# Optimization experiments

Measured on AMD Instinct MI355X. Metric: run time of the kernel, lower is better.

## Reference

```python
import jax, jax.numpy as jnp
import numpy as np

# Config (matches init_kwargs): range [-32,32]^3, voxel 0.5 -> 128^3 grid; BEV 200x200
PC_LOW = np.array([-32.0, -32.0, -32.0], dtype=np.float32)
PC_HIGH = np.array([32.0, 32.0, 32.0], dtype=np.float32)
VOX = 0.5
G = 128
BEV_H, BEV_W = 200, 200
BN_EPS = 1e-5
STRIDES = [1, 2, 1, 2, 1, 1]


def setup_inputs() -> dict:
    key = jax.random.key(0)
    ks = jax.random.split(key, 10)
    N = 2_000_000
    xyz = jax.random.uniform(ks[0], (N, 3), jnp.float32, minval=-32.0, maxval=32.0)
    inten = jax.random.uniform(ks[1], (N, 1), jnp.float32)
    points = jnp.concatenate([xyz, inten], axis=1)  # (N,4)
    chans = [(32, 4), (64, 32), (64, 64), (128, 64), (128, 128), (256, 128)]
    inp = {"points": points}
    for i, (co, ci) in enumerate(chans):
        fan_in = ci * 27
        inp[f"w{i+1}"] = jax.random.normal(ks[2 + i], (co, ci, 3, 3, 3), jnp.float32) / np.sqrt(fan_in)
        inp[f"g{i+1}"] = jnp.ones((co,), jnp.float32)
        inp[f"b{i+1}"] = jnp.zeros((co,), jnp.float32)
    return inp


def _voxelize(points):
    # range filtering + floor-binning + clamp, faithful to voxelize_points (dense path: scatter-ADD)
    low = jnp.asarray(PC_LOW)
    high = jnp.asarray(PC_HIGH)
    mask = jnp.all((points[:, :3] >= low) & (points[:, :3] <= high), axis=1)
    coords = jnp.floor((points[:, :3] - low) / VOX).astype(jnp.int32)
    coords = jnp.clip(coords, 0, G - 1)
    vals = points * mask[:, None].astype(points.dtype)  # invalid points contribute 0
    # original indexes voxel_grid[:, z, y, x]
    grid = jnp.zeros((G, G, G, 4), points.dtype)
    grid = grid.at[coords[:, 2], coords[:, 1], coords[:, 0]].add(vals)
    return jnp.transpose(grid, (3, 0, 1, 2))  # (4, G, G, G)


def _conv3d(x, w, s):
    # PyTorch Conv3d(k=3, padding=1, stride=s), NCDHW
    return jax.lax.conv_general_dilated(
        x, w, window_strides=(s, s, s), padding=[(1, 1), (1, 1), (1, 1)],
        dimension_numbers=("NCDHW", "OIDHW", "NCDHW"))


def _bn_relu(x, g, b):
    # eval-mode BN: running_mean=0, running_var=1
    scale = (g / jnp.sqrt(1.0 + BN_EPS))[None, :, None, None, None]
    return jax.nn.relu(x * scale + b[None, :, None, None, None])


def reference(points, w1, w2, w3, w4, w5, w6,
              g1, g2, g3, g4, g5, g6,
              b1, b2, b3, b4, b5, b6):
    ws = [w1, w2, w3, w4, w5, w6]
    gs = [g1, g2, g3, g4, g5, g6]
    bs = [b1, b2, b3, b4, b5, b6]
    x = _voxelize(points)[None]  # (1,4,G,G,G)
    for w, g, b, s in zip(ws, gs, bs, STRIDES):
        x = _bn_relu(_conv3d(x, w, s), g, b)
    feat = x[0]  # (256, G/4, G/4, G/4)
    bev = jnp.max(feat, axis=2)  # torch.max(..., dim=2) on (C,D1,D2,D3) -> (C,D1,D3)
    # F.interpolate bilinear align_corners=False == jax.image.resize half-pixel bilinear
    bev = jax.image.resize(bev, (bev.shape[0], BEV_H, BEV_W), method="bilinear")
    return bev
```

## Files before the change

### kernel.cpp

```cpp
#include <hip/hip_runtime.h>
#include <hip/hip_fp16.h>
#include <cstdint>
#include <cstddef>

typedef __attribute__((ext_vector_type(8))) short short8;
typedef __attribute__((ext_vector_type(8))) _Float16 half8;
typedef __attribute__((ext_vector_type(16))) float f32x16;

__device__ __forceinline__ float bf2f(unsigned short u) { return __uint_as_float(((unsigned)u) << 16); }
__device__ __forceinline__ unsigned short f2bf(float f) {
    unsigned u = __float_as_uint(f);
    return (unsigned short)((u + 0x7fffu + ((u >> 16) & 1u)) >> 16);
}
__device__ __forceinline__ void sync_lds() {
    asm volatile("s_waitcnt lgkmcnt(0)\n\ts_barrier" ::: "memory");
}

static constexpr float BN_INV = 0.9999950000374997f;


__device__ __forceinline__ int vox_bucket(float4 p, bool& ok) {
    ok = !(p.x < -32.f || p.x > 32.f || p.y < -32.f || p.y > 32.f || p.z < -32.f || p.z > 32.f);
    int cy = min(max((int)floorf((p.y + 32.f) * 2.f), 0), 127);
    int cz = min(max((int)floorf((p.z + 32.f) * 2.f), 0), 127);
    return cz * 4 + (cy >> 5);
}

__global__ __launch_bounds__(256) void vox_count(const float4* __restrict__ pts,
                                                 int* __restrict__ cnt, int N) {
    __shared__ int h[512];
    for (int t = threadIdx.x; t < 512; t += 256) h[t] = 0;
    __syncthreads();
    int stride = gridDim.x * 256;
    for (int i = blockIdx.x * 256 + threadIdx.x; i < N; i += stride) {
        float4 p = pts[i];
        bool ok;
        int bk = vox_bucket(p, ok);
        if (ok) atomicAdd(&h[bk], 1);
    }
    __syncthreads();
    for (int t = threadIdx.x; t < 512; t += 256)
        if (h[t]) atomicAdd(&cnt[t], h[t]);
}

__global__ void vox_scan(const int* __restrict__ cnt, int* __restrict__ off,
                         int* __restrict__ cur) {
    __shared__ int c[512];
    int t = threadIdx.x;
    c[t] = cnt[t];
    __syncthreads();
    int s = 0;
    for (int i = 0; i < t; ++i) s += c[i];
    off[t] = s;
    cur[t] = s;
}

__global__ __launch_bounds__(256) void vox_scatter(const float4* __restrict__ pts,
                                                   int* __restrict__ cur,
                                                   float4* __restrict__ sorted, int N) {
    __shared__ int h[512];
    __shared__ int base[512];
    int b0 = blockIdx.x * 4096;
    for (int t = threadIdx.x; t < 512; t += 256) h[t] = 0;
    __syncthreads();
    float4 p[16];
    int bk[16];
#pragma unroll
    for (int j = 0; j < 16; ++j) {
        int i = b0 + j * 256 + threadIdx.x;
        bk[j] = -1;
        if (i < N) {
            p[j] = pts[i];
            bool ok;
            int b = vox_bucket(p[j], ok);
            if (ok) {
                bk[j] = b;
                atomicAdd(&h[b], 1);
            }
        }
    }
    __syncthreads();
    for (int t = threadIdx.x; t < 512; t += 256) {
        int n = h[t];
        base[t] = n ? atomicAdd(&cur[t], n) : 0;
        h[t] = 0;
    }
    __syncthreads();
#pragma unroll
    for (int j = 0; j < 16; ++j) {
        if (bk[j] >= 0) {
            int r = atomicAdd(&h[bk[j]], 1);
            sorted[base[bk[j]] + r] = p[j];
        }
    }
}

__global__ __launch_bounds__(256) void vox_accum(const float4* __restrict__ sorted,
                                                 const int* __restrict__ off,
                                                 const int* __restrict__ cnt,
                                                 __half2* __restrict__ grid) {
    __shared__ float s[32 * 128 * 4];
    for (int t = threadIdx.x; t < 16384; t += 256) s[t] = 0.f;
    __syncthreads();
    int bid = blockIdx.x;
    int bz = bid >> 2;
    int ylo = (bid & 3) << 5;
    int b = off[bid], n = cnt[bid];
    for (int i = threadIdx.x; i < n; i += 256) {
        float4 p = sorted[b + i];
        int cx = min(max((int)floorf((p.x + 32.f) * 2.f), 0), 127);
        int cy = min(max((int)floorf((p.y + 32.f) * 2.f), 0), 127);
        float* v = s + ((cy - ylo) * 128 + cx) * 4;
        unsafeAtomicAdd(v + 0, p.x);
        unsafeAtomicAdd(v + 1, p.y);
        unsafeAtomicAdd(v + 2, p.z);
        unsafeAtomicAdd(v + 3, p.w);
    }
    __syncthreads();
    for (int t = threadIdx.x; t < 4096; t += 256) {
        int ry = t >> 7, cx = t & 127;
        const float* v = s + t * 4;
        union { __half2 h[2]; float2 f; } u;
        u.h[0] = __floats2half2_rn(v[0], v[1]);
        u.h[1] = __floats2half2_rn(v[2], v[3]);
        int gi = (((bz + 1) * 130 + (ylo + ry + 1)) * 130 + (cx + 1)) * 2;
        *(float2*)(grid + gi) = u.f;
    }
}

__global__ __launch_bounds__(256) void repack_w(const float* __restrict__ w, const float* __restrict__ g,
                                                unsigned short* __restrict__ o, int Co, int CI) {
    int i = blockIdx.x * 256 + threadIdx.x;
    int total = 27 * Co * CI;
    if (i >= total) return;
    int ci = i % CI;
    int t = i / CI;
    int co = t % Co;
    int k = t / Co;
    float v = w[((size_t)(co * CI + ci)) * 27 + k] * g[co] * BN_INV;
    o[i] = f2bf(v);
}
__global__ __launch_bounds__(256) void repack_w1m(const float* __restrict__ w, const float* __restrict__ g,
                                                  unsigned short* __restrict__ o) {
    int i = blockIdx.x * 256 + threadIdx.x;
    if (i >= 9 * 32 * 16) return;
    int k16 = i & 15;
    int co = (i >> 4) & 31;
    int p = i >> 9;
    float v = 0.f;
    if (k16 < 12) {
        int dx = k16 >> 2, ci = k16 & 3;
        int dz = p / 3, dy = p % 3;
        v = w[(co * 4 + ci) * 27 + dz * 9 + dy * 3 + dx] * g[co] * BN_INV;
    }
    o[i] = __half_as_ushort(__float2half(v));
}

__global__ __launch_bounds__(256) void conv1_mfma(
    const unsigned short* __restrict__ in, const unsigned short* __restrict__ wa,
    const float* __restrict__ beta, unsigned short* __restrict__ out,
    int zstart, int r0) {
    const int tid = threadIdx.x;
    const int l31 = tid & 31;
    const int lh = (tid >> 5) & 1;
    const int wv = tid >> 6;
    int v = blockIdx.x * 128 + wv * 32 + l31;
    int x = v & 127;
    int y = (v >> 7) & 127;
    int z = zstart + (v >> 14);

    const unsigned short* base = in + ((z * 130 + y) * 130 + x) * 4 + lh * 8;
    uint2 d0[9], d1[9];
    half8 a[9];
#pragma unroll
    for (int p = 0; p < 9; ++p) {
        int dz = p / 3, dy = p % 3;
        const unsigned short* rp = base + (dz * 130 + dy) * 520;
        d0[p] = *(const uint2*)(rp);
        d1[p] = *(const uint2*)(rp + 4);
        a[p] = *(const half8*)(wa + (p * 32 + l31) * 16 + lh * 8);
    }
    f32x16 acc = {0.f};
#pragma unroll
    for (int p = 0; p < 9; ++p) {
        uint4 braw = {d0[p].x, d0[p].y, d1[p].x, d1[p].y};
        half8 b = *(half8*)&braw;
        acc = __builtin_amdgcn_mfma_f32_32x32x16_f16(a[p], b, acc, 0, 0, 0);
    }
    int r = z - zstart + r0;
    int ob = ((r * 130 + (y + 1)) * 130 + (x + 1)) * 32;
#pragma unroll
    for (int g = 0; g < 4; ++g) {
        int cb = 4 * lh + 8 * g;
        float4 bt = *(const float4*)(beta + cb);
        ushort4 u;
        u.x = f2bf(fmaxf(acc[g * 4 + 0] + bt.x, 0.f));
        u.y = f2bf(fmaxf(acc[g * 4 + 1] + bt.y, 0.f));
        u.z = f2bf(fmaxf(acc[g * 4 + 2] + bt.z, 0.f));
        u.w = f2bf(fmaxf(acc[g * 4 + 3] + bt.w, 0.f));
        *(ushort4*)(out + ob + cb) = u;
    }
}

template <int CI, int KC, int S>
__global__ __launch_bounds__(256) void conv_mfma(
    const unsigned short* __restrict__ in, const unsigned short* __restrict__ wb,
    const float* __restrict__ beta, unsigned short* __restrict__ out,
    int D, int lgD, int Xp, int Xpo, int Co, int zin_base, int v_off) {

    constexpr int KCp = KC + 8;
    constexpr int OPB = KC / 8;
    constexpr int NB = KC / 16;
    constexpr int NA = KC / 32;
    constexpr int NCH = KC / 16;
    constexpr int NCC = CI / KC;
    constexpr int STOT = 27 * NCC;

    __shared__ __align__(16) short sA[2 * 64 * KCp];
    __shared__ __align__(16) short sB[2 * 128 * KCp];

    const int tid = threadIdx.x;
    const int l31 = tid & 31;
    const int lh = (tid >> 5) & 1;
    const int wv = tid >> 6;

    const unsigned gx = gridDim.x;
    const unsigned lin = blockIdx.y * gx + blockIdx.x;
    const unsigned q = (gx * gridDim.y) >> 3;
    const unsigned lin2 = (lin & 7) * q + (lin >> 3);
    const unsigned bxs = lin2 % gx;
    const unsigned bys = lin2 / gx;
    const int co0 = bxs * 64;

    int bgIdx[NB], blB[NB];
#pragma unroll
    for (int j = 0; j < NB; ++j) {
        int idx = tid + j * 256;
        int vL = idx / OPB;
        int oct = idx - vL * OPB;
        int vg = v_off + bys * 128 + vL;
        int x = vg & (D - 1);
        int ry = vg >> lgD;
        int y = ry & (D - 1);
        int z = ry >> lgD;
        bgIdx[j] = ((z * S * Xp + y * S) * Xp + x * S) * CI + oct * 8;
        blB[j] = vL * KCp + oct * 8;
    }
    int agIdx[NA], alA[NA];
#pragma unroll
    for (int j = 0; j < NA; ++j) {
        int idx = tid + j * 256;
        int cA = idx / OPB;
        int oct = idx - cA * OPB;
        agIdx[j] = (co0 + cA) * CI + oct * 8;
        alA[j] = cA * KCp + oct * 8;
    }
    const int bfr = (wv * 32 + l31) * KCp + lh * 8;
    const int afr = l31 * KCp + lh * 8;

    short8 rB[2][NB], rA[2][NA];

    auto loadStage = [&](int s, int r) {
        int k = s / NCC;
        int c0 = (s - k * NCC) * KC;
        int dz = k / 9;
        int rr = k - dz * 9;
        int dy = rr / 3;
        int dx = rr - dy * 3;
        int kb = (((dz - zin_base) * Xp + dy) * Xp + dx) * CI + c0;
        int ka = k * Co * CI + c0;
#pragma unroll
        for (int j = 0; j < NB; ++j) rB[r][j] = *(const short8*)(in + bgIdx[j] + kb);
#pragma unroll
        for (int j = 0; j < NA; ++j) rA[r][j] = *(const short8*)(wb + agIdx[j] + ka);
    };
    auto storeLDS = [&](int r, int buf) {
#pragma unroll
        for (int j = 0; j < NB; ++j) *(short8*)(sB + buf * 128 * KCp + blB[j]) = rB[r][j];
#pragma unroll
        for (int j = 0; j < NA; ++j) *(short8*)(sA + buf * 64 * KCp + alA[j]) = rA[r][j];
    };

    f32x16 acc0 = {0.f}, acc1 = {0.f};

    loadStage(0, 0);
    loadStage(1, 1);
    storeLDS(0, 0);
    sync_lds();

#pragma unroll
    for (int s = 0; s < STOT; ++s) {
        if (s + 2 < STOT) loadStage(s + 2, s & 1);
        const short* pB = sB + (s & 1) * 128 * KCp + bfr;
        const short* pA = sA + (s & 1) * 64 * KCp + afr;
#pragma unroll
        for (int c = 0; c < NCH; ++c) {
            short8 bv = *(const short8*)(pB + c * 16);
            short8 a0 = *(const short8*)(pA + c * 16);
            short8 a1 = *(const short8*)(pA + 32 * KCp + c * 16);
            acc0 = __builtin_amdgcn_mfma_f32_32x32x16_bf16(a0, bv, acc0, 0, 0, 0);
            acc1 = __builtin_amdgcn_mfma_f32_32x32x16_bf16(a1, bv, acc1, 0, 0, 0);
        }
        if (s + 1 < STOT) {
            storeLDS((s + 1) & 1, (s + 1) & 1);
            sync_lds();
        }
    }

    int vg = v_off + bys * 128 + wv * 32 + l31;
    int x = vg & (D - 1);
    int ry = vg >> lgD;
    int y = ry & (D - 1);
    int z = ry >> lgD;
    size_t ob = (((size_t)(z + 1) * Xpo + (y + 1)) * Xpo + (x + 1)) * Co + co0;
#pragma unroll
    for (int cot = 0; cot < 2; ++cot) {
        const f32x16& a = cot ? acc1 : acc0;
#pragma unroll
        for (int g = 0; g < 4; ++g) {
            int cb = cot * 32 + 4 * lh + 8 * g;
            float4 bt = *(const float4*)(beta + co0 + cb);
            ushort4 u;
            u.x = f2bf(fmaxf(a[g * 4 + 0] + bt.x, 0.f));
            u.y = f2bf(fmaxf(a[g * 4 + 1] + bt.y, 0.f));
            u.z = f2bf(fmaxf(a[g * 4 + 2] + bt.z, 0.f));
            u.w = f2bf(fmaxf(a[g * 4 + 3] + bt.w, 0.f));
            *(ushort4*)(out + ob + cb) = u;
        }
    }
}

__global__ __launch_bounds__(256) void bev_max_kernel(const unsigned short* __restrict__ feat,
                                                      float* __restrict__ bev) {
    int z = blockIdx.x >> 5;
    int x = blockIdx.x & 31;
    int c = threadIdx.x;
    const unsigned short* p = feat + ((((z + 1) * 34) + 1) * 34 + (x + 1)) * 256 + c;
    float mx = 0.f;
#pragma unroll
    for (int y = 0; y < 32; ++y) mx = fmaxf(mx, bf2f(p[y * 34 * 256]));
    bev[(z * 32 + x) * 256 + c] = mx;
}

__global__ __launch_bounds__(256) void resize_kernel(const float* __restrict__ bev,
                                                     float* __restrict__ out) {
    int i = blockIdx.x * 256 + threadIdx.x;
    if (i >= 256 * 200 * 200) return;
    int ox = i % 200;
    int t = i / 200;
    int oy = t % 200;
    int c = t / 200;
    const float sc = 32.0f / 200.0f;
    float fy = (oy + 0.5f) * sc - 0.5f;
    float fx = (ox + 0.5f) * sc - 0.5f;
    float fy0 = floorf(fy), fx0 = floorf(fx);
    float ty = fy - fy0, tx = fx - fx0;
    int y0 = min(max((int)fy0, 0), 31), y1 = min(max((int)fy0 + 1, 0), 31);
    int x0 = min(max((int)fx0, 0), 31), x1 = min(max((int)fx0 + 1, 0), 31);
    float v00 = bev[(y0 * 32 + x0) * 256 + c], v01 = bev[(y0 * 32 + x1) * 256 + c];
    float v10 = bev[(y1 * 32 + x0) * 256 + c], v11 = bev[(y1 * 32 + x1) * 256 + c];
    float top = v00 + tx * (v01 - v00);
    float bot = v10 + tx * (v11 - v10);
    out[i] = top + ty * (bot - top);
}

extern "C" void kernel_launch(void* const* d_in, const int* in_sizes, int n_in,
                              void* d_out, int out_size, void* d_ws, size_t ws_size,
                              hipStream_t stream) {
    const float* points = (const float*)d_in[0];
    int N = in_sizes[0] / 4;
    const float *W[6], *G[6], *B[6];
    for (int i = 0; i < 6; ++i) {
        W[i] = (const float*)d_in[1 + 3 * i];
        G[i] = (const float*)d_in[2 + 3 * i];
        B[i] = (const float*)d_in[3 + 3 * i];
    }

    char* ws = (char*)d_ws;
    const size_t MiB = 1ull << 20;
    unsigned short* gridH = (unsigned short*)(ws);
    int* cnt = (int*)(ws + 17580032);
    int* off = cnt + 512;
    int* cur = off + 512;
    float4* sorted = (float4*)(ws + 18 * MiB);
    unsigned short* O1s = (unsigned short*)(ws + 18 * MiB);
    unsigned short* O2p = (unsigned short*)(ws + 104 * MiB);
    unsigned short* O3p = (unsigned short*)(ws);
    unsigned short* O4p = (unsigned short*)(ws + 37 * MiB);
    unsigned short* O5p = (unsigned short*)(ws + 48 * MiB);
    unsigned short* O6p = (unsigned short*)(ws + 59 * MiB);
    float* bev = (float*)(ws + 80 * MiB);
    unsigned short* wc1 = (unsigned short*)(ws + 140 * MiB);
    unsigned short* wb2 = (unsigned short*)(ws + 140 * MiB + 16384);
    unsigned short* wb3 = wb2 + 27 * 64 * 32;
    unsigned short* wb4 = wb3 + 27 * 64 * 64;
    unsigned short* wb5 = wb4 + 27 * 128 * 64;
    unsigned short* wb6 = wb5 + 27 * 128 * 128;

    repack_w1m<<<18, 256, 0, stream>>>(W[0], G[0], wc1);
    repack_w<<<216, 256, 0, stream>>>(W[1], G[1], wb2, 64, 32);
    repack_w<<<432, 256, 0, stream>>>(W[2], G[2], wb3, 64, 64);
    repack_w<<<864, 256, 0, stream>>>(W[3], G[3], wb4, 128, 64);
    repack_w<<<1728, 256, 0, stream>>>(W[4], G[4], wb5, 128, 128);
    repack_w<<<3456, 256, 0, stream>>>(W[5], G[5], wb6, 256, 128);

    hipMemsetAsync(gridH, 0, 17576000, stream);
    hipMemsetAsync(cnt, 0, 2048, stream);
    hipMemsetAsync(O2p, 0, 36799488, stream);
    vox_count<<<1024, 256, 0, stream>>>((const float4*)points, cnt, N);
    vox_scan<<<1, 512, 0, stream>>>(cnt, off, cur);
    vox_scatter<<<(N + 4095) / 4096, 256, 0, stream>>>((const float4*)points, cur, sorted, N);
    vox_accum<<<512, 256, 0, stream>>>(sorted, off, cnt, (__half2*)gridH);

    hipMemsetAsync(O1s, 0, 70304000, stream);
    conv1_mfma<<<8192, 256, 0, stream>>>(gridH, wc1, B[0], O1s, 0, 1);
    conv_mfma<32, 32, 2><<<dim3(1, 1024), 256, 0, stream>>>(O1s, wb2, B[1], O2p, 64, 6, 130, 66, 64, 0, 0);
    conv1_mfma<<<8320, 256, 0, stream>>>(gridH, wc1, B[0], O1s, 63, 0);
    conv_mfma<32, 32, 2><<<dim3(1, 1024), 256, 0, stream>>>(O1s, wb2, B[1], O2p, 64, 6, 130, 66, 64, 64, 131072);

    hipMemsetAsync(O3p, 0, 36799488, stream);
    hipMemsetAsync(O4p, 0, 10061824, stream);
    hipMemsetAsync(O5p, 0, 10061824, stream);
    hipMemsetAsync(O6p, 0, 20123648, stream);

    conv_mfma<64, 64, 1><<<dim3(1, 2048), 256, 0, stream>>>(O2p, wb3, B[2], O3p, 64, 6, 66, 66, 64, 0, 0);
    conv_mfma<64, 64, 2><<<dim3(2, 256), 256, 0, stream>>>(O3p, wb4, B[3], O4p, 32, 5, 66, 34, 128, 0, 0);
    conv_mfma<128, 64, 1><<<dim3(2, 256), 256, 0, stream>>>(O4p, wb5, B[4], O5p, 32, 5, 34, 34, 128, 0, 0);
    conv_mfma<128, 64, 1><<<dim3(4, 256), 256, 0, stream>>>(O5p, wb6, B[5], O6p, 32, 5, 34, 34, 256, 0, 0);

    bev_max_kernel<<<1024, 256, 0, stream>>>(O6p, bev);
    resize_kernel<<<40000, 256, 0, stream>>>(bev, (float*)d_out);
}
```

Before: 686.7 us.

## Enlarge conv tiles to 64x64 per wave with 2x2 MFMA register blocking

Generalizes the implicit-GEMM conv kernel to template block sizes over output channels and voxels. Each wave now computes a 64x64 tile with four accumulators, reusing each A and B fragment twice, and the K chunk is fixed at 32. Layers get larger blocks (e.g. 64x256 or 128x128), halving grid sizes, plus launch-bounds occupancy hints and partial unrolling for long stage loops. The aim is fewer LDS reads and global loads per MFMA; the cost is more registers, less occupancy and fewer blocks, which may hurt small layers.

```diff
diff --git a/kernel.cpp b/kernel.cpp
--- a/kernel.cpp
+++ b/kernel.cpp
@@ -202,27 +202,30 @@
     }
 }
 
-template <int CI, int KC, int S>
-__global__ __launch_bounds__(256) void conv_mfma(
+template <int CI, int BCO, int BVX, int S, int MINW>
+__global__ __launch_bounds__(256, MINW) void conv_mfma(
     const unsigned short* __restrict__ in, const unsigned short* __restrict__ wb,
     const float* __restrict__ beta, unsigned short* __restrict__ out,
     int D, int lgD, int Xp, int Xpo, int Co, int zin_base, int v_off) {
 
+    constexpr int KC = 32;
     constexpr int KCp = KC + 8;
     constexpr int OPB = KC / 8;
-    constexpr int NB = KC / 16;
-    constexpr int NA = KC / 32;
-    constexpr int NCH = KC / 16;
+    constexpr int NB = BVX * KC / (256 * 8);
+    constexpr int NA = BCO * KC / (256 * 8);
     constexpr int NCC = CI / KC;
     constexpr int STOT = 27 * NCC;
-
-    __shared__ __align__(16) short sA[2 * 64 * KCp];
-    __shared__ __align__(16) short sB[2 * 128 * KCp];
+    constexpr int WVX = BVX / 64;
+
+    __shared__ __align__(16) short sA[2 * BCO * KCp];
+    __shared__ __align__(16) short sB[2 * BVX * KCp];
 
     const int tid = threadIdx.x;
     const int l31 = tid & 31;
     const int lh = (tid >> 5) & 1;
     const int wv = tid >> 6;
+    const int voxW = (wv & (WVX - 1)) * 64;
+    const int coW = (wv / WVX) * 64;
 
     const unsigned gx = gridDim.x;
     const unsigned lin = blockIdx.y * gx + blockIdx.x;
@@ -230,7 +233,7 @@
     const unsigned lin2 = (lin & 7) * q + (lin >> 3);
     const unsigned bxs = lin2 % gx;
     const unsigned bys = lin2 / gx;
-    const int co0 = bxs * 64;
+    const int co0 = bxs * BCO;
 
     int bgIdx[NB], blB[NB];
 #pragma unroll
@@ -238,7 +241,7 @@
         int idx = tid + j * 256;
         int vL = idx / OPB;
         int oct = idx - vL * OPB;
-        int vg = v_off + bys * 128 + vL;
+        int vg = v_off + bys * BVX + vL;
         int x = vg & (D - 1);
         int ry = vg >> lgD;
         int y = ry & (D - 1);
@@ -255,8 +258,8 @@
         agIdx[j] = (co0 + cA) * CI + oct * 8;
         alA[j] = cA * KCp + oct * 8;
     }
-    const int bfr = (wv * 32 + l31) * KCp + lh * 8;
-    const int afr = l31 * KCp + lh * 8;
+    const int aoff = (coW + l31) * KCp + lh * 8;
+    const int boff = (voxW + l31) * KCp + lh * 8;
 
     short8 rB[2][NB], rA[2][NA];
 
@@ -276,56 +279,69 @@
     };
     auto storeLDS = [&](int r, int buf) {
 #pragma unroll
-        for (int j = 0; j < NB; ++j) *(short8*)(sB + buf * 128 * KCp + blB[j]) = rB[r][j];
-#pragma unroll
-        for (int j = 0; j < NA; ++j) *(short8*)(sA + buf * 64 * KCp + alA[j]) = rA[r][j];
+        for (int j = 0; j < NB; ++j) *(short8*)(sB + buf * BVX * KCp + blB[j]) = rB[r][j];
+#pragma unroll
+        for (int j = 0; j < NA; ++j) *(short8*)(sA + buf * BCO * KCp + alA[j]) = rA[r][j];
     };
 
-    f32x16 acc0 = {0.f}, acc1 = {0.f};
+    f32x16 acc00 = {0.f}, acc01 = {0.f}, acc10 = {0.f}, acc11 = {0.f};
 
     loadStage(0, 0);
     loadStage(1, 1);
     storeLDS(0, 0);
     sync_lds();
 
-#pragma unroll
-    for (int s = 0; s < STOT; ++s) {
+    auto stage = [&](int s) {
         if (s + 2 < STOT) loadStage(s + 2, s & 1);
-        const short* pB = sB + (s & 1) * 128 * KCp + bfr;
-        const short* pA = sA + (s & 1) * 64 * KCp + afr;
-#pragma unroll
-        for (int c = 0; c < NCH; ++c) {
-            short8 bv = *(const short8*)(pB + c * 16);
-            short8 a0 = *(const short8*)(pA + c * 16);
-            short8 a1 = *(const short8*)(pA + 32 * KCp + c * 16);
-            acc0 = __builtin_amdgcn_mfma_f32_32x32x16_bf16(a0, bv, acc0, 0, 0, 0);
-            acc1 = __builtin_amdgcn_mfma_f32_32x32x16_bf16(a1, bv, acc1, 0, 0, 0);
+        const short* pB = sB + (s & 1) * BVX * KCp;
+        const short* pA = sA + (s & 1) * BCO * KCp;
+#pragma unroll
+        for (int c = 0; c < 2; ++c) {
+            short8 a0 = *(const short8*)(pA + aoff + c * 16);
+            short8 a1 = *(const short8*)(pA + aoff + 32 * KCp + c * 16);
+            short8 b0 = *(const short8*)(pB + boff + c * 16);
+            short8 b1 = *(const short8*)(pB + boff + 32 * KCp + c * 16);
+            acc00 = __builtin_amdgcn_mfma_f32_32x32x16_bf16(a0, b0, acc00, 0, 0, 0);
+            acc01 = __builtin_amdgcn_mfma_f32_32x32x16_bf16(a0, b1, acc01, 0, 0, 0);
+            acc10 = __builtin_amdgcn_mfma_f32_32x32x16_bf16(a1, b0, acc10, 0, 0, 0);
+            acc11 = __builtin_amdgcn_mfma_f32_32x32x16_bf16(a1, b1, acc11, 0, 0, 0);
         }
         if (s + 1 < STOT) {
             storeLDS((s + 1) & 1, (s + 1) & 1);
             sync_lds();
         }
-    }
-
-    int vg = v_off + bys * 128 + wv * 32 + l31;
-    int x = vg & (D - 1);
-    int ry = vg >> lgD;
-    int y = ry & (D - 1);
-    int z = ry >> lgD;
-    size_t ob = (((size_t)(z + 1) * Xpo + (y + 1)) * Xpo + (x + 1)) * Co + co0;
-#pragma unroll
-    for (int cot = 0; cot < 2; ++cot) {
-        const f32x16& a = cot ? acc1 : acc0;
-#pragma unroll
-        for (int g = 0; g < 4; ++g) {
-            int cb = cot * 32 + 4 * lh + 8 * g;
-            float4 bt = *(const float4*)(beta + co0 + cb);
-            ushort4 u;
-            u.x = f2bf(fmaxf(a[g * 4 + 0] + bt.x, 0.f));
-            u.y = f2bf(fmaxf(a[g * 4 + 1] + bt.y, 0.f));
-            u.z = f2bf(fmaxf(a[g * 4 + 2] + bt.z, 0.f));
-            u.w = f2bf(fmaxf(a[g * 4 + 3] + bt.w, 0.f));
-            *(ushort4*)(out + ob + cb) = u;
+    };
+    if constexpr (STOT <= 54) {
+#pragma unroll
+        for (int s = 0; s < STOT; ++s) stage(s);
+    } else {
+#pragma unroll 2
+        for (int s = 0; s < STOT; ++s) stage(s);
+    }
+
+#pragma unroll
+    for (int i = 0; i < 2; ++i) {
+#pragma unroll
+        for (int j = 0; j < 2; ++j) {
+            const f32x16& a = (i == 0) ? (j == 0 ? acc00 : acc01) : (j == 0 ? acc10 : acc11);
+            int vg2 = v_off + bys * BVX + voxW + j * 32 + l31;
+            int x = vg2 & (D - 1);
+            int ry = vg2 >> lgD;
+            int y = ry & (D - 1);
+            int z = ry >> lgD;
+            int cbase = co0 + coW + i * 32;
+            size_t ob = (((size_t)(z + 1) * Xpo + (y + 1)) * Xpo + (x + 1)) * Co + cbase;
+#pragma unroll
+            for (int g = 0; g < 4; ++g) {
+                int cb = 4 * lh + 8 * g;
+                float4 bt = *(const float4*)(beta + cbase + cb);
+                ushort4 u;
+                u.x = f2bf(fmaxf(a[g * 4 + 0] + bt.x, 0.f));
+                u.y = f2bf(fmaxf(a[g * 4 + 1] + bt.y, 0.f));
+                u.z = f2bf(fmaxf(a[g * 4 + 2] + bt.z, 0.f));
+                u.w = f2bf(fmaxf(a[g * 4 + 3] + bt.w, 0.f));
+                *(ushort4*)(out + ob + cb) = u;
+            }
         }
     }
 }
@@ -414,19 +430,19 @@
 
     hipMemsetAsync(O1s, 0, 70304000, stream);
     conv1_mfma<<<8192, 256, 0, stream>>>(gridH, wc1, B[0], O1s, 0, 1);
-    conv_mfma<32, 32, 2><<<dim3(1, 1024), 256, 0, stream>>>(O1s, wb2, B[1], O2p, 64, 6, 130, 66, 64, 0, 0);
+    conv_mfma<32, 64, 256, 2, 3><<<dim3(1, 512), 256, 0, stream>>>(O1s, wb2, B[1], O2p, 64, 6, 130, 66, 64, 0, 0);
     conv1_mfma<<<8320, 256, 0, stream>>>(gridH, wc1, B[0], O1s, 63, 0);
-    conv_mfma<32, 32, 2><<<dim3(1, 1024), 256, 0, stream>>>(O1s, wb2, B[1], O2p, 64, 6, 130, 66, 64, 64, 131072);
+    conv_mfma<32, 64, 256, 2, 3><<<dim3(1, 512), 256, 0, stream>>>(O1s, wb2, B[1], O2p, 64, 6, 130, 66, 64, 64, 131072);
 
     hipMemsetAsync(O3p, 0, 36799488, stream);
     hipMemsetAsync(O4p, 0, 10061824, stream);
     hipMemsetAsync(O5p, 0, 10061824, stream);
     hipMemsetAsync(O6p, 0, 20123648, stream);
 
-    conv_mfma<64, 64, 1><<<dim3(1, 2048), 256, 0, stream>>>(O2p, wb3, B[2], O3p, 64, 6, 66, 66, 64, 0, 0);
-    conv_mfma<64, 64, 2><<<dim3(2, 256), 256, 0, stream>>>(O3p, wb4, B[3], O4p, 32, 5, 66, 34, 128, 0, 0);
-    conv_mfma<128, 64, 1><<<dim3(2, 256), 256, 0, stream>>>(O4p, wb5, B[4], O5p, 32, 5, 34, 34, 128, 0, 0);
-    conv_mfma<128, 64, 1><<<dim3(4, 256), 256, 0, stream>>>(O5p, wb6, B[5], O6p, 32, 5, 34, 34, 256, 0, 0);
+    conv_mfma<64, 64, 256, 1, 3><<<dim3(1, 1024), 256, 0, stream>>>(O2p, wb3, B[2], O3p, 64, 6, 66, 66, 64, 0, 0);
+    conv_mfma<64, 128, 128, 2, 4><<<dim3(1, 256), 256, 0, stream>>>(O3p, wb4, B[3], O4p, 32, 5, 66, 34, 128, 0, 0);
+    conv_mfma<128, 128, 128, 1, 4><<<dim3(1, 256), 256, 0, stream>>>(O4p, wb5, B[4], O5p, 32, 5, 34, 34, 128, 0, 0);
+    conv_mfma<128, 128, 128, 1, 4><<<dim3(2, 256), 256, 0, stream>>>(O5p, wb6, B[5], O6p, 32, 5, 34, 34, 256, 0, 0);
 
     bev_max_kernel<<<1024, 256, 0, stream>>>(O6p, bev);
     resize_kernel<<<40000, 256, 0, stream>>>(bev, (float*)d_out);
```

Result: slower. 746.6 us (+8.7%).

## Load activation B-fragments directly from global into registers, bypassing LDS

Applied to the files above, without the earlier changes.

The conv_mfma kernel no longer stages input activations through shared memory. Each lane now reads its own voxel's channel fragments straight from global memory into registers and feeds them to MFMA, which removes the sB buffer and its LDS stores and reads. Only weights still go through LDS. A launch-bounds occupancy hint of 4 blocks is also added. In exchange, global reads are per-lane strided, 16-byte accesses with no cooperative coalescing, and B prefetch depth drops to one stage.

```diff
diff --git a/kernel.cpp b/kernel.cpp
--- a/kernel.cpp
+++ b/kernel.cpp
@@ -203,21 +203,19 @@
 }
 
 template <int CI, int KC, int S>
-__global__ __launch_bounds__(256) void conv_mfma(
+__global__ __launch_bounds__(256, 4) void conv_mfma(
     const unsigned short* __restrict__ in, const unsigned short* __restrict__ wb,
     const float* __restrict__ beta, unsigned short* __restrict__ out,
     int D, int lgD, int Xp, int Xpo, int Co, int zin_base, int v_off) {
 
     constexpr int KCp = KC + 8;
     constexpr int OPB = KC / 8;
-    constexpr int NB = KC / 16;
     constexpr int NA = KC / 32;
     constexpr int NCH = KC / 16;
     constexpr int NCC = CI / KC;
     constexpr int STOT = 27 * NCC;
 
     __shared__ __align__(16) short sA[2 * 64 * KCp];
-    __shared__ __align__(16) short sB[2 * 128 * KCp];
 
     const int tid = threadIdx.x;
     const int l31 = tid & 31;
@@ -232,20 +230,15 @@
     const unsigned bys = lin2 / gx;
     const int co0 = bxs * 64;
 
-    int bgIdx[NB], blB[NB];
-#pragma unroll
-    for (int j = 0; j < NB; ++j) {
-        int idx = tid + j * 256;
-        int vL = idx / OPB;
-        int oct = idx - vL * OPB;
-        int vg = v_off + bys * 128 + vL;
-        int x = vg & (D - 1);
-        int ry = vg >> lgD;
-        int y = ry & (D - 1);
-        int z = ry >> lgD;
-        bgIdx[j] = ((z * S * Xp + y * S) * Xp + x * S) * CI + oct * 8;
-        blB[j] = vL * KCp + oct * 8;
-    }
+    const int vg = v_off + bys * 128 + wv * 32 + l31;
+    {
+    }
+    const int xx = vg & (D - 1);
+    const int ryy = vg >> lgD;
+    const int yy = ryy & (D - 1);
+    const int zz = ryy >> lgD;
+    const int bIdx = ((zz * S * Xp + yy * S) * Xp + xx * S) * CI + lh * 8;
+
     int agIdx[NA], alA[NA];
 #pragma unroll
     for (int j = 0; j < NA; ++j) {
@@ -255,64 +248,67 @@
         agIdx[j] = (co0 + cA) * CI + oct * 8;
         alA[j] = cA * KCp + oct * 8;
     }
-    const int bfr = (wv * 32 + l31) * KCp + lh * 8;
     const int afr = l31 * KCp + lh * 8;
 
-    short8 rB[2][NB], rA[2][NA];
-
-    auto loadStage = [&](int s, int r) {
+    short8 rA[2][NA];
+    short8 rB[2][NCH];
+
+    auto tapOff = [&](int s, int& kb, int& ka) {
         int k = s / NCC;
         int c0 = (s - k * NCC) * KC;
         int dz = k / 9;
         int rr = k - dz * 9;
         int dy = rr / 3;
         int dx = rr - dy * 3;
-        int kb = (((dz - zin_base) * Xp + dy) * Xp + dx) * CI + c0;
-        int ka = k * Co * CI + c0;
-#pragma unroll
-        for (int j = 0; j < NB; ++j) rB[r][j] = *(const short8*)(in + bgIdx[j] + kb);
+        kb = (((dz - zin_base) * Xp + dy) * Xp + dx) * CI + c0;
+        ka = k * Co * CI + c0;
+    };
+    auto loadA = [&](int s, int r) {
+        int kb, ka;
+        tapOff(s, kb, ka);
 #pragma unroll
         for (int j = 0; j < NA; ++j) rA[r][j] = *(const short8*)(wb + agIdx[j] + ka);
     };
-    auto storeLDS = [&](int r, int buf) {
-#pragma unroll
-        for (int j = 0; j < NB; ++j) *(short8*)(sB + buf * 128 * KCp + blB[j]) = rB[r][j];
+    auto loadB = [&](int s, int r) {
+        int kb, ka;
+        tapOff(s, kb, ka);
+        const unsigned short* bp = in + bIdx + kb;
+#pragma unroll
+        for (int c = 0; c < NCH; ++c) rB[r][c] = *(const short8*)(bp + c * 16);
+    };
+    auto storeA = [&](int r, int buf) {
 #pragma unroll
         for (int j = 0; j < NA; ++j) *(short8*)(sA + buf * 64 * KCp + alA[j]) = rA[r][j];
     };
 
     f32x16 acc0 = {0.f}, acc1 = {0.f};
 
-    loadStage(0, 0);
-    loadStage(1, 1);
-    storeLDS(0, 0);
+    loadA(0, 0);
+    loadA(1, 1);
+    loadB(0, 0);
+    storeA(0, 0);
     sync_lds();
 
 #pragma unroll
     for (int s = 0; s < STOT; ++s) {
-        if (s + 2 < STOT) loadStage(s + 2, s & 1);
-        const short* pB = sB + (s & 1) * 128 * KCp + bfr;
+        if (s + 2 < STOT) loadA(s + 2, s & 1);
+        if (s + 1 < STOT) loadB(s + 1, (s + 1) & 1);
         const short* pA = sA + (s & 1) * 64 * KCp + afr;
 #pragma unroll
         for (int c = 0; c < NCH; ++c) {
-            short8 bv = *(const short8*)(pB + c * 16);
+            short8 bv = rB[s & 1][c];
             short8 a0 = *(const short8*)(pA + c * 16);
             short8 a1 = *(const short8*)(pA + 32 * KCp + c * 16);
             acc0 = __builtin_amdgcn_mfma_f32_32x32x16_bf16(a0, bv, acc0, 0, 0, 0);
             acc1 = __builtin_amdgcn_mfma_f32_32x32x16_bf16(a1, bv, acc1, 0, 0, 0);
         }
         if (s + 1 < STOT) {
-            storeLDS((s + 1) & 1, (s + 1) & 1);
+            storeA((s + 1) & 1, (s + 1) & 1);
             sync_lds();
         }
     }
 
-    int vg = v_off + bys * 128 + wv * 32 + l31;
-    int x = vg & (D - 1);
-    int ry = vg >> lgD;
-    int y = ry & (D - 1);
-    int z = ry >> lgD;
-    size_t ob = (((size_t)(z + 1) * Xpo + (y + 1)) * Xpo + (x + 1)) * Co + co0;
+    size_t ob = (((size_t)(zz + 1) * Xpo + (yy + 1)) * Xpo + (xx + 1)) * Co + co0;
 #pragma unroll
     for (int cot = 0; cot < 2; ++cot) {
         const f32x16& a = cot ? acc1 : acc0;
```

New measurement: 821.2 us. 19.6% more time.
